# Kernel tuning notes

Measured on AMD Instinct MI355X. Metric: run time of the kernel, lower is better.

## Reference

```python
import jax, jax.numpy as jnp
import numpy as np

N, E, B = 20000, 640000, 4096
IN_DIM, HID, A, D, C = 128, 256, 8, 64, 2


def setup_inputs() -> dict:
    key = jax.random.key(0)
    ks = jax.random.split(key, 16)
    inp = {
        "feature": jax.random.normal(ks[0], (N, IN_DIM), dtype=jnp.float32),
        "src": jax.random.randint(ks[1], (E,), 0, N),
        "dst": jax.random.randint(ks[2], (E,), 0, N),
        "pairs": jax.random.randint(ks[3], (B, 2), 0, N),
        # gcn1.linear: in_dim -> hid
        "W1": jax.random.normal(ks[4], (HID, IN_DIM), dtype=jnp.float32) * 0.02,
        "b1": jnp.zeros((HID,), dtype=jnp.float32),
        # aspEmbed (no bias): hid -> A*D
        "aspW": jax.random.normal(ks[5], (A * D, HID), dtype=jnp.float32) * 0.02,
        # Aspect_Representation.linear: D -> 1
        "attW": jax.random.normal(ks[6], (1, D), dtype=jnp.float32) * 0.02,
        "attb": jnp.zeros((1,), dtype=jnp.float32),
        # aspect_merge_linear: D -> 1
        "mergeW": jax.random.normal(ks[7], (1, D), dtype=jnp.float32) * 0.02,
        "mergeb": jnp.zeros((1,), dtype=jnp.float32),
        # concat_linear: 2A -> C
        "catW": jax.random.normal(ks[8], (C, 2 * A), dtype=jnp.float32) * 0.02,
        "catb": jnp.zeros((C,), dtype=jnp.float32),
    }
    return inp


def _aspect_head(pe, aspW, attW, attb, mergeW, mergeb):
    # pe: [B, HID]
    b = pe.shape[0]
    asp = (pe @ aspW.T).reshape(b, A, D)               # [B, A, D]
    score = jax.nn.softmax(asp @ attW.T + attb, axis=1)  # [B, A, 1] softmax over aspects
    rep = score * asp                                   # [B, A, D]
    return (rep @ mergeW.T + mergeb)[..., 0]            # [B, A]


def reference(feature, src, dst, pairs, W1, b1, aspW, attW, attb,
              mergeW, mergeb, catW, catb):
    n = feature.shape[0]
    nf = feature + feature.mean(axis=0)                 # node_feature
    # GCNLayer: u_mul_v message + mean aggregation at dst
    msg = nf[src] * nf[dst]                             # [E, IN_DIM]
    agg = jax.ops.segment_sum(msg, dst, num_segments=n)
    deg = jax.ops.segment_sum(jnp.ones((msg.shape[0],), dtype=feature.dtype), dst, num_segments=n)
    x = agg / jnp.where(deg > 0, deg, 1.0)[:, None]
    x = x @ W1.T + b1                                   # [N, HID] (dropout = identity in eval)
    p1 = _aspect_head(x[pairs[:, 0]], aspW, attW, attb, mergeW, mergeb)
    p2 = _aspect_head(x[pairs[:, 1]], aspW, attW, attb, mergeW, mergeb)
    out = jnp.concatenate([p1, p2], axis=1) @ catW.T + catb  # [B, C]
    return jax.nn.log_softmax(out, axis=-1)
```

## Files before the change

### kernel.cpp

```cpp
#include <hip/hip_runtime.h>
#include <hip/hip_bf16.h>

constexpr int IN_DIM = 128;
constexpr int HID    = 256;
constexpr int A_     = 8;
constexpr int D_     = 64;
constexpr int PAD    = 128;
constexpr int NBITW  = 1024;

__global__ __launch_bounds__(1024) void k1_all(
    const float* __restrict__ aspW, const float* __restrict__ attW,
    const float* __restrict__ mergeW, const float* __restrict__ b1,
    const float* __restrict__ attb, const float* __restrict__ W1,
    const float* __restrict__ feat, const int* __restrict__ pairsFlat,
    float* __restrict__ WS, float* __restrict__ WM,
    float* __restrict__ sb, float* __restrict__ mb,
    unsigned int* __restrict__ bitsG, int* __restrict__ wl, int* __restrict__ wlcnt,
    ulonglong2* __restrict__ zbase, int n16,
    float* __restrict__ pb, int N, int nIdx) {
  __shared__ float smem[4096];
  const int bid = blockIdx.x;
  const int t = threadIdx.x;

  if (bid == 0) {
    unsigned int* bits = (unsigned int*)smem;
    __shared__ int cnt_l;
    if (t < NBITW) bits[t] = 0u;
    if (t == 0) cnt_l = 0;
    __syncthreads();
#pragma unroll
    for (int k = 0; k < 8; ++k) {
      int i = k * 1024 + t;
      if (i < nIdx) {
        int node = pairsFlat[i];
        unsigned int m = 1u << (node & 31);
        unsigned int old = atomicOr(&bits[node >> 5], m);
        if ((old & m) == 0u) {
          int p = atomicAdd(&cnt_l, 1);
          wl[p] = node;
        }
      }
    }
    __syncthreads();
    if (t < NBITW) bitsG[t] = bits[t];
    if (t == 0) *wlcnt = cnt_l;
    return;
  }
  if (bid <= A_) {
    int a = bid - 1;
    float* psS = smem;
    float* psM = smem + 1024;
    float* Us  = smem + 2048;
    float* Um  = smem + 2304;
    float* r1  = smem + 2560;
    float* r2  = smem + 2816;
    {
      int h = t & 255, dq = t >> 8;
      float ss = 0.f, sm = 0.f;
      const float* ap = aspW + (size_t)(a * D_ + dq * 16) * HID + h;
#pragma unroll
      for (int d = 0; d < 16; ++d) {
        float w = ap[(size_t)d * HID];
        ss += attW[dq * 16 + d] * w;
        sm += mergeW[dq * 16 + d] * w;
      }
      psS[dq * 256 + h] = ss;
      psM[dq * 256 + h] = sm;
    }
    __syncthreads();
    if (t < HID) {
      float us = psS[t] + psS[256 + t] + psS[512 + t] + psS[768 + t];
      float um = psM[t] + psM[256 + t] + psM[512 + t] + psM[768 + t];
      Us[t] = us; Um[t] = um;
      float bv = b1[t];
      r1[t] = us * bv; r2[t] = um * bv;
    }
    __syncthreads();
    for (int ofs = 128; ofs > 0; ofs >>= 1) {
      if (t < ofs) { r1[t] += r1[t + ofs]; r2[t] += r2[t + ofs]; }
      __syncthreads();
    }
    if (t == 0) { sb[a] = r1[0] + attb[0]; mb[a] = r2[0]; }
    __syncthreads();
    {
      int j = t & 127, ch = t >> 7;
      float ws = 0.f, wm = 0.f;
      const float* w1p = W1 + (size_t)(ch * 32) * IN_DIM + j;
      const float* usp = Us + ch * 32;
      const float* ump = Um + ch * 32;
#pragma unroll
      for (int k = 0; k < 32; ++k) {
        float w = w1p[(size_t)k * IN_DIM];
        ws += usp[k] * w;
        wm += ump[k] * w;
      }
      psS[ch * 128 + j] = ws;
      psM[ch * 128 + j] = wm;
    }
    __syncthreads();
    if (t < IN_DIM) {
      float ws = 0.f, wm = 0.f;
#pragma unroll
      for (int c = 0; c < 8; ++c) { ws += psS[c * 128 + t]; wm += psM[c * 128 + t]; }
      WS[a * IN_DIM + t] = ws;
      WM[a * IN_DIM + t] = wm;
    }
    return;
  }
  if (bid <= 16) {
    ulonglong2 z; z.x = 0ull; z.y = 0ull;
    for (int i = (bid - 9) * 1024 + t; i < n16; i += 8 * 1024) zbase[i] = z;
    return;
  }
  {
    int cb = bid - 17;
    int rslot = t >> 5, c4 = t & 31;
    int row = cb * 32 + rslot;
    float4 acc = make_float4(0.f, 0.f, 0.f, 0.f);
    if (row < N) {
      float4 v = ((const float4*)feat)[(size_t)row * 32 + c4];
      acc = v;
    }
    ((float4*)smem)[rslot * 32 + c4] = acc;
    __syncthreads();
    if (t < IN_DIM) {
      float s = 0.f;
#pragma unroll 8
      for (int r = 0; r < 32; ++r) s += smem[r * IN_DIM + t];
      pb[(size_t)cb * IN_DIM + t] = s;
    }
  }
}

__global__ void k2_fill_colred(const int4* __restrict__ src4, const int4* __restrict__ dst4,
                               const unsigned int* __restrict__ bitsG, int* __restrict__ cnt,
                               int* __restrict__ esrc, int E4, int fillBlocks,
                               const float* __restrict__ pb, float* __restrict__ colsum,
                               int npart) {
  if ((int)blockIdx.x >= fillBlocks) {
    int rblk = (int)blockIdx.x - fillBlocks;
    int t = threadIdx.x;
    float4 acc = make_float4(0.f, 0.f, 0.f, 0.f);
    for (int row = t; row < npart; row += 256) {
      float4 v = ((const float4*)(pb + (size_t)row * IN_DIM))[rblk];
      acc.x += v.x; acc.y += v.y; acc.z += v.z; acc.w += v.w;
    }
    __shared__ float4 red[256];
    red[t] = acc;
    __syncthreads();
    for (int ofs = 128; ofs > 0; ofs >>= 1) {
      if (t < ofs) {
        float4 o = red[t + ofs];
        red[t].x += o.x; red[t].y += o.y; red[t].z += o.z; red[t].w += o.w;
      }
      __syncthreads();
    }
    if (t == 0) ((float4*)colsum)[rblk] = red[0];
    return;
  }
  int e = blockIdx.x * blockDim.x + threadIdx.x;
  if (e >= E4) return;
  int4 d = dst4[e];
  int4 s = src4[e];
  if ((bitsG[d.x >> 5] >> (d.x & 31)) & 1u) { int p = atomicAdd(&cnt[d.x], 1); if (p < PAD) esrc[(size_t)d.x * PAD + p] = s.x; }
  if ((bitsG[d.y >> 5] >> (d.y & 31)) & 1u) { int p = atomicAdd(&cnt[d.y], 1); if (p < PAD) esrc[(size_t)d.y * PAD + p] = s.y; }
  if ((bitsG[d.z >> 5] >> (d.z & 31)) & 1u) { int p = atomicAdd(&cnt[d.z], 1); if (p < PAD) esrc[(size_t)d.z * PAD + p] = s.z; }
  if ((bitsG[d.w >> 5] >> (d.w & 31)) & 1u) { int p = atomicAdd(&cnt[d.w], 1); if (p < PAD) esrc[(size_t)d.w * PAD + p] = s.w; }
}

__global__ void __launch_bounds__(64) pull_k(
    const float* __restrict__ feat, const float* __restrict__ colsum,
    const int* __restrict__ cnt, const int* __restrict__ esrc,
    const int* __restrict__ wl, const int* __restrict__ wlcnt,
    const float* __restrict__ WS, const float* __restrict__ WM,
    float* __restrict__ nodevals, float invN) {
  int widx = blockIdx.x;
  if (widx >= *wlcnt) return;
  int d = wl[widx];
  int lane = threadIdx.x;
  int deg = cnt[d];
  const float2* F = (const float2*)feat;
  const int* es = esrc + (size_t)d * PAD;
  int n = deg < PAD ? deg : PAD;
  float2 acc = make_float2(0.f, 0.f);
  int i = 0;
  for (; i + 7 < n; i += 8) {
    float2 v0 = F[(size_t)es[i + 0] * 64 + lane];
    float2 v1 = F[(size_t)es[i + 1] * 64 + lane];
    float2 v2 = F[(size_t)es[i + 2] * 64 + lane];
    float2 v3 = F[(size_t)es[i + 3] * 64 + lane];
    float2 v4 = F[(size_t)es[i + 4] * 64 + lane];
    float2 v5 = F[(size_t)es[i + 5] * 64 + lane];
    float2 v6 = F[(size_t)es[i + 6] * 64 + lane];
    float2 v7 = F[(size_t)es[i + 7] * 64 + lane];
    acc.x += ((v0.x + v1.x) + (v2.x + v3.x)) + ((v4.x + v5.x) + (v6.x + v7.x));
    acc.y += ((v0.y + v1.y) + (v2.y + v3.y)) + ((v4.y + v5.y) + (v6.y + v7.y));
  }
  for (; i < n; ++i) {
    float2 v0 = F[(size_t)es[i] * 64 + lane];
    acc.x += v0.x;
    acc.y += v0.y;
  }
  float2 cm = ((const float2*)colsum)[lane];
  cm.x *= invN;
  cm.y *= invN;
  float2 fd = F[(size_t)d * 64 + lane];
  float2 x;
  if (deg > 0) {
    float inv = 1.0f / (float)deg;
    x.x = (fd.x + cm.x) * (acc.x * inv + cm.x);
    x.y = (fd.y + cm.y) * (acc.y * inv + cm.y);
  } else {
    x.x = 0.f;
    x.y = 0.f;
  }
  float v[16];
#pragma unroll
  for (int a = 0; a < A_; ++a) {
    float2 w = ((const float2*)WS)[a * 64 + lane];
    float2 u = ((const float2*)WM)[a * 64 + lane];
    v[a] = x.x * w.x + x.y * w.y;
    v[8 + a] = x.x * u.x + x.y * u.y;
  }
#pragma unroll
  for (int m = 32; m > 0; m >>= 1) {
#pragma unroll
    for (int k = 0; k < 16; ++k) v[k] += __shfl_xor(v[k], m, 64);
  }
  if (lane == 0) {
#pragma unroll
    for (int k = 0; k < 16; ++k) nodevals[(size_t)d * 16 + k] = v[k];
  }
}

__global__ void pair_k(const int* __restrict__ pairs, const float* __restrict__ nodevals,
                       const float* __restrict__ sb, const float* __restrict__ mb,
                       const float* __restrict__ catW, const float* __restrict__ catb,
                       const float* __restrict__ mergeb, float* __restrict__ out, int B) {
  int b = blockIdx.x * blockDim.x + threadIdx.x;
  if (b >= B) return;
  float mgb = mergeb[0];
  float p[2 * A_];
  for (int side = 0; side < 2; ++side) {
    int node = pairs[b * 2 + side];
    const float4* nv = (const float4*)(nodevals + (size_t)node * 16);
    float4 q0 = nv[0], q1 = nv[1], q2 = nv[2], q3 = nv[3];
    float s[A_] = {q0.x, q0.y, q0.z, q0.w, q1.x, q1.y, q1.z, q1.w};
    float m[A_] = {q2.x, q2.y, q2.z, q2.w, q3.x, q3.y, q3.z, q3.w};
#pragma unroll
    for (int a = 0; a < A_; ++a) { s[a] += sb[a]; m[a] += mb[a]; }
    float mx = s[0];
#pragma unroll
    for (int a = 1; a < A_; ++a) mx = fmaxf(mx, s[a]);
    float es[A_], sum = 0.f;
#pragma unroll
    for (int a = 0; a < A_; ++a) { es[a] = __expf(s[a] - mx); sum += es[a]; }
    float rsum = 1.0f / sum;
#pragma unroll
    for (int a = 0; a < A_; ++a) p[side * A_ + a] = es[a] * rsum * m[a] + mgb;
  }
  float o0 = catb[0], o1 = catb[1];
#pragma unroll
  for (int k = 0; k < 2 * A_; ++k) {
    o0 += p[k] * catW[k];
    o1 += p[k] * catW[2 * A_ + k];
  }
  float mx = fmaxf(o0, o1);
  float lse = mx + logf(__expf(o0 - mx) + __expf(o1 - mx));
  out[b * 2 + 0] = o0 - lse;
  out[b * 2 + 1] = o1 - lse;
}

extern "C" void kernel_launch(void* const* d_in, const int* in_sizes, int n_in,
                              void* d_out, int out_size, void* d_ws, size_t ws_size,
                              hipStream_t stream) {
  const float* feature = (const float*)d_in[0];
  const int*   src     = (const int*)d_in[1];
  const int*   dst     = (const int*)d_in[2];
  const int*   pairs   = (const int*)d_in[3];
  const float* W1      = (const float*)d_in[4];
  const float* b1      = (const float*)d_in[5];
  const float* aspW    = (const float*)d_in[6];
  const float* attW    = (const float*)d_in[7];
  const float* attb    = (const float*)d_in[8];
  const float* mergeW  = (const float*)d_in[9];
  const float* mergebp = (const float*)d_in[10];
  const float* catW    = (const float*)d_in[11];
  const float* catb    = (const float*)d_in[12];

  const int N = in_sizes[0] / IN_DIM;
  const int E = in_sizes[1];
  const int B = in_sizes[3] / 2;
  const int npart = (N + 31) / 32;
  const int fillBlocks = (E / 4 + 255) / 256;
  const int E4 = E / 4;

  char* ws = (char*)d_ws;
  size_t off_b = 0;
  int* cnt = (int*)(ws + off_b);        off_b += (size_t)N * sizeof(int);
  size_t zero_bytes = (off_b + 15) & ~(size_t)15;
  off_b = zero_bytes;
  unsigned int* bitsG = (unsigned int*)(ws + off_b); off_b += NBITW * sizeof(unsigned int);
  int* wlcnt = (int*)(ws + off_b);      off_b += 4 * sizeof(int);
  int* wl = (int*)(ws + off_b);         off_b += (size_t)(2 * B) * sizeof(int);
  float* colsum = (float*)(ws + off_b); off_b += IN_DIM * sizeof(float);
  float* pb = (float*)(ws + off_b);     off_b += (size_t)npart * IN_DIM * sizeof(float);
  float* WS = (float*)(ws + off_b);     off_b += A_ * IN_DIM * sizeof(float);
  float* WM = (float*)(ws + off_b);     off_b += A_ * IN_DIM * sizeof(float);
  float* sb = (float*)(ws + off_b);     off_b += A_ * sizeof(float);
  float* mb = (float*)(ws + off_b);     off_b += A_ * sizeof(float);
  float* nodevals = (float*)(ws + off_b); off_b += (size_t)N * 16 * sizeof(float);
  int* esrc = (int*)(ws + off_b);       off_b += (size_t)N * PAD * sizeof(int);

  k1_all<<<17 + npart, 1024, 0, stream>>>(
      aspW, attW, mergeW, b1, attb, W1, feature, pairs,
      WS, WM, sb, mb, bitsG, wl, wlcnt,
      (ulonglong2*)d_ws, (int)(zero_bytes / 16), pb, N, 2 * B);
  k2_fill_colred<<<fillBlocks + 32, 256, 0, stream>>>(
      (const int4*)src, (const int4*)dst, bitsG, cnt, esrc, E4, fillBlocks,
      pb, colsum, npart);
  pull_k<<<2 * B, 64, 0, stream>>>(feature, colsum, cnt, esrc, wl, wlcnt, WS, WM,
                                   nodevals, 1.0f / (float)N);
  pair_k<<<(B + 255) / 256, 256, 0, stream>>>(pairs, nodevals, sb, mb, catW, catb,
                                              mergebp, (float*)d_out, B);
}
```

Baseline: 49.20 us.

## Fuse node pull and pair head into one per-pair kernel, drop worklist

Removes the deduplicated worklist and the per-node nodevals buffer. A new kernel launches one block per pair, with two 64-lane waves each pulling one endpoint's neighbor features, then computes the aspect head and log-softmax in shared memory. This saves one kernel launch and the nodevals round trip through global memory, but nodes that appear in several pairs now have their aggregation recomputed.

```diff
diff --git a/kernel.cpp b/kernel.cpp
--- a/kernel.cpp
+++ b/kernel.cpp
@@ -15,7 +15,7 @@
     const float* __restrict__ feat, const int* __restrict__ pairsFlat,
     float* __restrict__ WS, float* __restrict__ WM,
     float* __restrict__ sb, float* __restrict__ mb,
-    unsigned int* __restrict__ bitsG, int* __restrict__ wl, int* __restrict__ wlcnt,
+    unsigned int* __restrict__ bitsG,
     ulonglong2* __restrict__ zbase, int n16,
     float* __restrict__ pb, int N, int nIdx) {
   __shared__ float smem[4096];
@@ -24,26 +24,18 @@
 
   if (bid == 0) {
     unsigned int* bits = (unsigned int*)smem;
-    __shared__ int cnt_l;
     if (t < NBITW) bits[t] = 0u;
-    if (t == 0) cnt_l = 0;
     __syncthreads();
 #pragma unroll
     for (int k = 0; k < 8; ++k) {
       int i = k * 1024 + t;
       if (i < nIdx) {
         int node = pairsFlat[i];
-        unsigned int m = 1u << (node & 31);
-        unsigned int old = atomicOr(&bits[node >> 5], m);
-        if ((old & m) == 0u) {
-          int p = atomicAdd(&cnt_l, 1);
-          wl[p] = node;
-        }
+        atomicOr(&bits[node >> 5], 1u << (node & 31));
       }
     }
     __syncthreads();
     if (t < NBITW) bitsG[t] = bits[t];
-    if (t == 0) *wlcnt = cnt_l;
     return;
   }
   if (bid <= A_) {
@@ -168,16 +160,19 @@
   if ((bitsG[d.w >> 5] >> (d.w & 31)) & 1u) { int p = atomicAdd(&cnt[d.w], 1); if (p < PAD) esrc[(size_t)d.w * PAD + p] = s.w; }
 }
 
-__global__ void __launch_bounds__(64) pull_k(
+__global__ void __launch_bounds__(128) pairhead_k(
     const float* __restrict__ feat, const float* __restrict__ colsum,
     const int* __restrict__ cnt, const int* __restrict__ esrc,
-    const int* __restrict__ wl, const int* __restrict__ wlcnt,
-    const float* __restrict__ WS, const float* __restrict__ WM,
-    float* __restrict__ nodevals, float invN) {
-  int widx = blockIdx.x;
-  if (widx >= *wlcnt) return;
-  int d = wl[widx];
-  int lane = threadIdx.x;
+    const int* __restrict__ pairsFlat, const float* __restrict__ WS,
+    const float* __restrict__ WM, const float* __restrict__ sb,
+    const float* __restrict__ mb, const float* __restrict__ catW,
+    const float* __restrict__ catb, const float* __restrict__ mergeb,
+    float* __restrict__ out, float invN) {
+  __shared__ float pv[2][16];
+  int b = blockIdx.x;
+  int side = threadIdx.x >> 6;
+  int lane = threadIdx.x & 63;
+  int d = pairsFlat[2 * b + side];
   int deg = cnt[d];
   const float2* F = (const float2*)feat;
   const int* es = esrc + (size_t)d * PAD;
@@ -229,46 +224,38 @@
   }
   if (lane == 0) {
 #pragma unroll
-    for (int k = 0; k < 16; ++k) nodevals[(size_t)d * 16 + k] = v[k];
-  }
-}
-
-__global__ void pair_k(const int* __restrict__ pairs, const float* __restrict__ nodevals,
-                       const float* __restrict__ sb, const float* __restrict__ mb,
-                       const float* __restrict__ catW, const float* __restrict__ catb,
-                       const float* __restrict__ mergeb, float* __restrict__ out, int B) {
-  int b = blockIdx.x * blockDim.x + threadIdx.x;
-  if (b >= B) return;
-  float mgb = mergeb[0];
-  float p[2 * A_];
-  for (int side = 0; side < 2; ++side) {
-    int node = pairs[b * 2 + side];
-    const float4* nv = (const float4*)(nodevals + (size_t)node * 16);
-    float4 q0 = nv[0], q1 = nv[1], q2 = nv[2], q3 = nv[3];
-    float s[A_] = {q0.x, q0.y, q0.z, q0.w, q1.x, q1.y, q1.z, q1.w};
-    float m[A_] = {q2.x, q2.y, q2.z, q2.w, q3.x, q3.y, q3.z, q3.w};
-#pragma unroll
-    for (int a = 0; a < A_; ++a) { s[a] += sb[a]; m[a] += mb[a]; }
-    float mx = s[0];
-#pragma unroll
-    for (int a = 1; a < A_; ++a) mx = fmaxf(mx, s[a]);
-    float es[A_], sum = 0.f;
-#pragma unroll
-    for (int a = 0; a < A_; ++a) { es[a] = __expf(s[a] - mx); sum += es[a]; }
-    float rsum = 1.0f / sum;
-#pragma unroll
-    for (int a = 0; a < A_; ++a) p[side * A_ + a] = es[a] * rsum * m[a] + mgb;
-  }
-  float o0 = catb[0], o1 = catb[1];
-#pragma unroll
-  for (int k = 0; k < 2 * A_; ++k) {
-    o0 += p[k] * catW[k];
-    o1 += p[k] * catW[2 * A_ + k];
-  }
-  float mx = fmaxf(o0, o1);
-  float lse = mx + logf(__expf(o0 - mx) + __expf(o1 - mx));
-  out[b * 2 + 0] = o0 - lse;
-  out[b * 2 + 1] = o1 - lse;
+    for (int k = 0; k < 16; ++k) pv[side][k] = v[k];
+  }
+  __syncthreads();
+  if (threadIdx.x == 0) {
+    float mgb = mergeb[0];
+    float p[2 * A_];
+#pragma unroll
+    for (int sd = 0; sd < 2; ++sd) {
+      float s[A_], m[A_];
+#pragma unroll
+      for (int a = 0; a < A_; ++a) { s[a] = pv[sd][a] + sb[a]; m[a] = pv[sd][8 + a] + mb[a]; }
+      float mx = s[0];
+#pragma unroll
+      for (int a = 1; a < A_; ++a) mx = fmaxf(mx, s[a]);
+      float es_[A_], sum = 0.f;
+#pragma unroll
+      for (int a = 0; a < A_; ++a) { es_[a] = __expf(s[a] - mx); sum += es_[a]; }
+      float rsum = 1.0f / sum;
+#pragma unroll
+      for (int a = 0; a < A_; ++a) p[sd * A_ + a] = es_[a] * rsum * m[a] + mgb;
+    }
+    float o0 = catb[0], o1 = catb[1];
+#pragma unroll
+    for (int k = 0; k < 2 * A_; ++k) {
+      o0 += p[k] * catW[k];
+      o1 += p[k] * catW[2 * A_ + k];
+    }
+    float mx = fmaxf(o0, o1);
+    float lse = mx + logf(__expf(o0 - mx) + __expf(o1 - mx));
+    out[b * 2 + 0] = o0 - lse;
+    out[b * 2 + 1] = o1 - lse;
+  }
 }
 
 extern "C" void kernel_launch(void* const* d_in, const int* in_sizes, int n_in,
@@ -301,26 +288,22 @@
   size_t zero_bytes = (off_b + 15) & ~(size_t)15;
   off_b = zero_bytes;
   unsigned int* bitsG = (unsigned int*)(ws + off_b); off_b += NBITW * sizeof(unsigned int);
-  int* wlcnt = (int*)(ws + off_b);      off_b += 4 * sizeof(int);
-  int* wl = (int*)(ws + off_b);         off_b += (size_t)(2 * B) * sizeof(int);
   float* colsum = (float*)(ws + off_b); off_b += IN_DIM * sizeof(float);
   float* pb = (float*)(ws + off_b);     off_b += (size_t)npart * IN_DIM * sizeof(float);
   float* WS = (float*)(ws + off_b);     off_b += A_ * IN_DIM * sizeof(float);
   float* WM = (float*)(ws + off_b);     off_b += A_ * IN_DIM * sizeof(float);
   float* sb = (float*)(ws + off_b);     off_b += A_ * sizeof(float);
   float* mb = (float*)(ws + off_b);     off_b += A_ * sizeof(float);
-  float* nodevals = (float*)(ws + off_b); off_b += (size_t)N * 16 * sizeof(float);
   int* esrc = (int*)(ws + off_b);       off_b += (size_t)N * PAD * sizeof(int);
 
   k1_all<<<17 + npart, 1024, 0, stream>>>(
       aspW, attW, mergeW, b1, attb, W1, feature, pairs,
-      WS, WM, sb, mb, bitsG, wl, wlcnt,
+      WS, WM, sb, mb, bitsG,
       (ulonglong2*)d_ws, (int)(zero_bytes / 16), pb, N, 2 * B);
   k2_fill_colred<<<fillBlocks + 32, 256, 0, stream>>>(
       (const int4*)src, (const int4*)dst, bitsG, cnt, esrc, E4, fillBlocks,
       pb, colsum, npart);
-  pull_k<<<2 * B, 64, 0, stream>>>(feature, colsum, cnt, esrc, wl, wlcnt, WS, WM,
-                                   nodevals, 1.0f / (float)N);
-  pair_k<<<(B + 255) / 256, 256, 0, stream>>>(pairs, nodevals, sb, mb, catW, catb,
-                                              mergebp, (float*)d_out, B);
+  pairhead_k<<<B, 128, 0, stream>>>(feature, colsum, cnt, esrc, pairs, WS, WM,
+                                    sb, mb, catW, catb, mergebp, (float*)d_out,
+                                    1.0f / (float)N);
 }
```

Result: no change. 49.86 us (+1.3%).
